# Kernel optimization log

Hardware: AMD Instinct MI355X
Metric: run time of the kernel (lower is better)

The kernel has to match this reference:

```python
import jax, jax.numpy as jnp
import numpy as np

SHAPE = (128, 128, 128)  # (D, H, W), batch_size = 1
N = 100000               # number of active voxels
CONV_CH = [(3, 64), (64, 64), (64, 96), (96, 96), (96, 128), (128, 128),
           (128, 160), (160, 160), (160, 192), (192, 192), (192, 224),
           (224, 224), (224, 256), (256, 256)]


def _lin(c, shape):
    Sz, Sy, Sx = shape
    return ((c[:, 0] * Sz + c[:, 1]) * Sy + c[:, 2]) * Sx + c[:, 3]


def _subm_pairs(coords, shape):
    # Submanifold conv indice pairs: for each active voxel and each of the
    # 27 kernel offsets, the row index of the active neighbor, or -1.
    Sz, Sy, Sx = shape
    n = coords.shape[0]
    grid = np.full(Sz * Sy * Sx, -1, np.int64)  # batch size 1 dense lookup (like self.grid)
    grid[_lin(coords, shape)] = np.arange(n)
    pairs = []
    for dz in (-1, 0, 1):
        for dy in (-1, 0, 1):
            for dx in (-1, 0, 1):
                z = coords[:, 1] + dz
                y = coords[:, 2] + dy
                x = coords[:, 3] + dx
                ok = (z >= 0) & (z < Sz) & (y >= 0) & (y < Sy) & (x >= 0) & (x < Sx)
                nl = ((coords[:, 0] * Sz + z) * Sy + y) * Sx + x
                pairs.append(np.where(ok, grid[np.clip(nl, 0, grid.size - 1)], -1))
    return np.stack(pairs)  # [27, n]


def _pool_structure(coords, shape):
    # SparseMaxPool3d(2,2): output sites = unique coords//2; inv maps each
    # input voxel to its output window.
    ns = tuple(s // 2 for s in shape)
    c2 = coords.copy()
    c2[:, 1:] = c2[:, 1:] // 2
    key = _lin(c2, ns)
    uniq, inv = np.unique(key, return_inverse=True)
    Sz, Sy, Sx = ns
    b = uniq // (Sz * Sy * Sx)
    r = uniq % (Sz * Sy * Sx)
    z = r // (Sy * Sx)
    r = r % (Sy * Sx)
    nc = np.stack([b, z, r // Sx, r % Sx], 1).astype(np.int64)
    return nc, inv, uniq.shape[0], ns


def _build_plan(coors_np):
    # Paired SubMConv3d layers share an indice_key -> same pairs per level.
    coords = coors_np.astype(np.int64)
    shape = SHAPE
    plan = []
    for lvl in range(7):
        p = jnp.asarray(_subm_pairs(coords, shape))
        plan.append(('conv', p))
        plan.append(('conv', p))
        if lvl < 6:
            coords, inv, m, shape = _pool_structure(coords, shape)
            plan.append(('pool', jnp.asarray(inv), m))
    return plan


def _subm_conv(feats, pairs, W):
    # gather -> GEMM -> accumulate, per kernel offset (W: [27, Cin, Cout])
    out = jnp.zeros((feats.shape[0], W.shape[2]), feats.dtype)
    for k in range(27):
        idx = pairs[k]
        g = jnp.where((idx >= 0)[:, None], feats[jnp.clip(idx, 0)], 0.0)
        out = out + g @ W[k]
    return out


def _forward(feats, weights, plan):
    wi = 0
    for step in plan:
        if step[0] == 'conv':
            feats = _subm_conv(feats, step[1], weights[wi])
            wi += 1
        else:
            feats = jax.ops.segment_max(feats, step[1], num_segments=step[2])
    return feats


def setup_inputs() -> dict:
    rng = np.random.default_rng(0)
    lin = rng.choice(SHAPE[0] * SHAPE[1] * SHAPE[2], size=N, replace=False)
    z = lin // (SHAPE[1] * SHAPE[2])
    r = lin % (SHAPE[1] * SHAPE[2])
    coors = np.stack([np.zeros(N, np.int32), z.astype(np.int32),
                      (r // SHAPE[2]).astype(np.int32), (r % SHAPE[2]).astype(np.int32)], 1)
    key = jax.random.key(0)
    keys = jax.random.split(key, len(CONV_CH) + 1)
    inp = {
        'features': jax.random.normal(keys[0], (N, 3), jnp.float32),
        'coors': jnp.asarray(coors),
        'batch_size': 1,
    }
    for i, (ci, co) in enumerate(CONV_CH):
        inp[f'w{i}'] = jax.random.normal(keys[i + 1], (27, ci, co), jnp.float32) * (1.0 / np.sqrt(27.0 * ci))
    return inp


def reference(features, coors, batch_size, w0, w1, w2, w3, w4, w5, w6, w7, w8, w9, w10, w11, w12, w13):
    plan = _build_plan(np.asarray(coors))
    ws = [w0, w1, w2, w3, w4, w5, w6, w7, w8, w9, w10, w11, w12, w13]
    return _forward(features, ws, plan)
```

## Files before the change

### kernel.cpp

```cpp
#include <hip/hip_runtime.h>
#include <cstdint>
#include <cstddef>


typedef __attribute__((ext_vector_type(8))) short short8v;
typedef __attribute__((ext_vector_type(4))) float f32x4;

static inline int cdiv_h(int a, int b) { return (a + b - 1) / b; }

__device__ inline unsigned short f2bf(float f) {
    unsigned int u = __builtin_bit_cast(unsigned int, f);
    u += 0x7FFFu + ((u >> 16) & 1u);
    return (unsigned short)(u >> 16);
}
__device__ inline float bf2f(unsigned short h) {
    unsigned int u = ((unsigned int)h) << 16;
    return __builtin_bit_cast(float, u);
}

__device__ inline void gload_lds16(const void* g, void* l) {
    auto gp = (const __attribute__((address_space(1))) unsigned int*)(uintptr_t)g;
    auto lp = (__attribute__((address_space(3))) unsigned int*)(uintptr_t)l;
    __builtin_amdgcn_global_load_lds(gp, lp, 16, 0, 0);
}

__device__ inline int xcd_swz(int bid, int nwg) {
    int q = nwg >> 3, r = nwg & 7;
    int x = bid & 7, idx = bid >> 3;
    return (x < r ? x * (q + 1) : r * (q + 1) + (x - r) * q) + idx;
}

__global__ void set_count_k(int* counts, int n) { counts[0] = n; }

__global__ void scatter_grid_k(const int* __restrict__ coords, const int* __restrict__ cnt,
                               int* __restrict__ grid, int S)
{
    int i = blockIdx.x * blockDim.x + threadIdx.x;
    if (i >= cnt[0]) return;
    int z = coords[i * 4 + 1], y = coords[i * 4 + 2], x = coords[i * 4 + 3];
    grid[(z * S + y) * S + x] = i;
}

__global__ void build_pairs_k(const int* __restrict__ coords, const int* __restrict__ cnt,
                              const int* __restrict__ grid, int* __restrict__ pairs_t, int S)
{
    int i = blockIdx.x * blockDim.x + threadIdx.x;
    if (i >= cnt[0]) return;
    int z = coords[i * 4 + 1], y = coords[i * 4 + 2], x = coords[i * 4 + 3];
    int4* dst = reinterpret_cast<int4*>(pairs_t + (size_t)i * 32);
#pragma unroll
    for (int g = 0; g < 7; ++g) {
        int4 q;
#pragma unroll
        for (int j = 0; j < 4; ++j) {
            int k = g * 4 + j;
            int v = -1;
            if (k < 27) {
                int nz = z + k / 9 - 1;
                int ny = y + (k / 3) % 3 - 1;
                int nx = x + k % 3 - 1;
                if (nz >= 0 && nz < S && ny >= 0 && ny < S && nx >= 0 && nx < S)
                    v = grid[(nz * S + ny) * S + nx];
            }
            ((int*)&q)[j] = v;
        }
        dst[g] = q;
    }
}

struct PackArgs {
    const float* src[13];
    unsigned short* dst[13];
    int cin[13];
    int cout[13];
    int tileStart[14];
};

__global__ __launch_bounds__(256) void pack_all_k(PackArgs pa)
{
    int g = blockIdx.x * 4 + ((int)threadIdx.x >> 6);
    int lane = (int)threadIdx.x & 63;
    if (g >= pa.tileStart[13]) return;
    int li = 0;
    while (li < 12 && g >= pa.tileStart[li + 1]) ++li;
    int tile = g - pa.tileStart[li];
    int CIN = pa.cin[li], COUT = pa.cout[li];
    int NS = CIN >> 5, NT = COUT >> 4;
    int t = tile % NT;
    int s = (tile / NT) % NS;
    int k = tile / (NT * NS);
    int kabs = s * 32 + (lane >> 4) * 8;
    int c = t * 16 + (lane & 15);
    const float* src = pa.src[li] + ((size_t)(k * CIN + kabs)) * COUT + c;
    unsigned short* dst = pa.dst[li] + (size_t)tile * 512 + lane * 8;
#pragma unroll
    for (int j = 0; j < 8; ++j) dst[j] = f2bf(src[(size_t)j * COUT]);
}

__global__ __launch_bounds__(256) void conv0_k(
    const float* __restrict__ fin, const float* __restrict__ W,
    const int* __restrict__ pairs_t, const int* __restrict__ cnt,
    unsigned short* __restrict__ fout)
{
    const int row = blockIdx.x * 16 + ((int)threadIdx.x >> 4);
    const int cg = ((int)threadIdx.x & 15) * 4;
    if (row >= cnt[0]) return;
    float a0 = 0, a1 = 0, a2 = 0, a3 = 0;
    for (int k = 0; k < 27; ++k) {
        int nb = pairs_t[(size_t)row * 32 + k];
        if (nb < 0) continue;
        const float* fr = fin + (size_t)nb * 3;
        const float* wk = W + (size_t)k * 3 * 64 + cg;
#pragma unroll
        for (int ci = 0; ci < 3; ++ci) {
            float f = fr[ci];
            float4 w = *reinterpret_cast<const float4*>(wk + ci * 64);
            a0 += f * w.x; a1 += f * w.y; a2 += f * w.z; a3 += f * w.w;
        }
    }
    size_t o = (size_t)row * 64 + cg;
    fout[o] = f2bf(a0); fout[o + 1] = f2bf(a1);
    fout[o + 2] = f2bf(a2); fout[o + 3] = f2bf(a3);
}

template <int CIN, int COUT, int RT, int CT, int GY, bool OUTF32>
__global__ __launch_bounds__(256) void conv_lds_k(
    const unsigned short* __restrict__ fin, const unsigned short* __restrict__ Wp,
    const int* __restrict__ pairs_t, const int* __restrict__ cnt,
    void* __restrict__ fout)
{
    constexpr int NS = CIN / 32, NT = COUT / 16;
    constexpr int NCH = NS * CT;
    __shared__ unsigned short sB[2][NCH * 512];

    const int lane = (int)threadIdx.x & 63;
    const int wave = (int)threadIdx.x >> 6;
    const int l15 = lane & 15, lhi = lane >> 4;
    const int M = cnt[0];

    const int lid = xcd_swz((int)blockIdx.x, (int)gridDim.x);
    const int rowBlock = lid / GY;
    const int ct0 = (lid % GY) * CT;
    const int rowBase = (rowBlock * 4 + wave) * (RT * 16);

    const unsigned short* __restrict__ finL = fin + (size_t)lhi * 8;

    f32x4 acc[RT][CT];
#pragma unroll
    for (int a = 0; a < RT; ++a)
#pragma unroll
        for (int b = 0; b < CT; ++b) acc[a][b] = (f32x4){0.f, 0.f, 0.f, 0.f};

    int  rowC[RT];
    bool rOK[RT];
#pragma unroll
    for (int rt = 0; rt < RT; ++rt) {
        int r = rowBase + rt * 16 + l15;
        rOK[rt]  = r < M;
        rowC[rt] = rOK[rt] ? r : 0;
    }

#define STAGE(K, BUF)                                                              \
    {                                                                              \
        const unsigned short* srcB = Wp + (size_t)(K) * (NS * NT * 512)            \
                                     + (size_t)lane * 8;                           \
        _Pragma("unroll") for (int ii = 0; ii < (NCH + 3) / 4; ++ii) {             \
            int idx = wave + ii * 4;                                               \
            if (idx < NCH) {                                                       \
                int s = idx / CT, tt = idx % CT;                                   \
                gload_lds16(srcB + ((size_t)s * NT + ct0 + tt) * 512,              \
                            &sB[BUF][idx * 512]);                                  \
            }                                                                      \
        }                                                                          \
    }

    int nbCur[RT], nbNxt[RT];
#pragma unroll
    for (int rt = 0; rt < RT; ++rt)
        nbCur[rt] = rOK[rt] ? pairs_t[(size_t)rowC[rt] * 32 + 0] : -1;

    STAGE(0, 0);

    for (int k = 0; k < 27; ++k) {
        __syncthreads();
        if (k < 26) {
            STAGE(k + 1, (k + 1) & 1);
#pragma unroll
            for (int rt = 0; rt < RT; ++rt)
                nbNxt[rt] = rOK[rt] ? pairs_t[(size_t)rowC[rt] * 32 + (k + 1)] : -1;
        }

        int nb[RT], act[RT];
        bool anyAct = false;
#pragma unroll
        for (int rt = 0; rt < RT; ++rt) {
            nb[rt] = nbCur[rt];
            act[rt] = __any(nb[rt] >= 0);
            anyAct = anyAct || (act[rt] != 0);
        }
#pragma unroll
        for (int rt = 0; rt < RT; ++rt) nbCur[rt] = nbNxt[rt];

        if (anyAct) {
            const unsigned short* __restrict__ buf = sB[k & 1];
            short8v afr[NS][RT];
#pragma unroll
            for (int s = 0; s < NS; ++s)
#pragma unroll
                for (int rt = 0; rt < RT; ++rt) {
                    afr[s][rt] = (short8v){};
                    if (nb[rt] >= 0)
                        afr[s][rt] = *reinterpret_cast<const short8v*>(
                            finL + (size_t)nb[rt] * CIN + s * 32);
                }
#pragma unroll
            for (int s = 0; s < NS; ++s) {
                short8v bb[CT];
#pragma unroll
                for (int t = 0; t < CT; ++t)
                    bb[t] = *reinterpret_cast<const short8v*>(
                        &buf[(s * CT + t) * 512 + lane * 8]);
#pragma unroll
                for (int rt = 0; rt < RT; ++rt) {
                    if (!act[rt]) continue;
#pragma unroll
                    for (int t = 0; t < CT; ++t)
                        acc[rt][t] = __builtin_amdgcn_mfma_f32_16x16x32_bf16(
                            afr[s][rt], bb[t], acc[rt][t], 0, 0, 0);
                }
            }
        }
    }
#undef STAGE

#pragma unroll
    for (int rt = 0; rt < RT; ++rt) {
#pragma unroll
        for (int j = 0; j < 4; ++j) {
            int r = rowBase + rt * 16 + lhi * 4 + j;
            if (r >= M) continue;
#pragma unroll
            for (int t = 0; t < CT; ++t) {
                int c = (ct0 + t) * 16 + l15;
                if constexpr (OUTF32)
                    ((float*)fout)[(size_t)r * COUT + c] = acc[rt][t][j];
                else
                    ((unsigned short*)fout)[(size_t)r * COUT + c] = f2bf(acc[rt][t][j]);
            }
        }
    }
}

template <int CIN, int COUT, int CTD, int TG>
__global__ __launch_bounds__(64) void conv_deep_k(
    const unsigned short* __restrict__ fin, const unsigned short* __restrict__ Wp,
    const int* __restrict__ pairs_t, const int* __restrict__ cnt,
    float* __restrict__ fout)
{
    constexpr int NS = CIN / 32, NT = COUT / 16;
    const int lane = (int)threadIdx.x;
    const int l15 = lane & 15, lhi = lane >> 4;
    const int M = cnt[0];
    if ((int)blockIdx.x * 16 >= M) return;
    const int row = blockIdx.x * 16 + l15;
    const int ct0 = blockIdx.y * CTD;
    const int k0 = blockIdx.z * TG;

    f32x4 acc[CTD];
#pragma unroll
    for (int t = 0; t < CTD; ++t) acc[t] = (f32x4){0.f, 0.f, 0.f, 0.f};

    bool anyTap = false;
#pragma unroll
    for (int kk = 0; kk < TG; ++kk) {
        const int k = k0 + kk;
        int nb = (row < M) ? pairs_t[(size_t)row * 32 + k] : -1;
        if (!__any(nb >= 0)) continue;
        anyTap = true;
        const unsigned short* wk = Wp + (size_t)k * NS * NT * 512 + (size_t)lane * 8;
#pragma unroll
        for (int s = 0; s < NS; ++s) {
            short8v a = (short8v){};
            if (nb >= 0)
                a = *reinterpret_cast<const short8v*>(
                    fin + (size_t)nb * CIN + s * 32 + lhi * 8);
#pragma unroll
            for (int t = 0; t < CTD; ++t) {
                short8v b = *reinterpret_cast<const short8v*>(
                    wk + ((size_t)s * NT + ct0 + t) * 512);
                acc[t] = __builtin_amdgcn_mfma_f32_16x16x32_bf16(a, b, acc[t], 0, 0, 0);
            }
        }
    }
    if (!anyTap) return;

#pragma unroll
    for (int t = 0; t < CTD; ++t)
#pragma unroll
        for (int j = 0; j < 4; ++j) {
            int r = blockIdx.x * 16 + lhi * 4 + j;
            if (r < M)
                atomicAdd(&fout[(size_t)r * COUT + (ct0 + t) * 16 + l15], acc[t][j]);
        }
}

__global__ __launch_bounds__(256) void f32_to_bf16_k(
    const float* __restrict__ src, const int* __restrict__ cnt,
    unsigned short* __restrict__ dst, int C)
{
    int idx = blockIdx.x * 256 + (int)threadIdx.x;
    if (idx / C >= cnt[0]) return;
    dst[idx] = f2bf(src[idx]);
}

__global__ void mark_occ_k(const int* __restrict__ coords, const int* __restrict__ cnt,
                           int* __restrict__ occ, int Sh)
{
    int i = blockIdx.x * blockDim.x + threadIdx.x;
    if (i >= cnt[0]) return;
    int z = coords[i * 4 + 1] >> 1, y = coords[i * 4 + 2] >> 1, x = coords[i * 4 + 3] >> 1;
    occ[(z * Sh + y) * Sh + x] = 1;
}

__global__ __launch_bounds__(256) void scan_sum_k(const int* __restrict__ occ, int P,
                                                  int* __restrict__ bsum)
{
    int base = blockIdx.x * 4096 + (int)threadIdx.x * 16;
    int s = 0;
#pragma unroll
    for (int j = 0; j < 16; ++j) { int i = base + j; s += (i < P) ? occ[i] : 0; }
    for (int off = 1; off < 64; off <<= 1) s += __shfl_xor(s, off);
    __shared__ int ws[4];
    if ((threadIdx.x & 63) == 0) ws[threadIdx.x >> 6] = s;
    __syncthreads();
    if (threadIdx.x == 0) bsum[blockIdx.x] = ws[0] + ws[1] + ws[2] + ws[3];
}

__global__ void scan_offsets_k(const int* __restrict__ bsum, int nb,
                               int* __restrict__ boff, int* __restrict__ cntOut)
{
    int lane = threadIdx.x;
    int v = (lane < nb) ? bsum[lane] : 0;
    int incl = v;
    for (int off = 1; off < 64; off <<= 1) {
        int t = __shfl_up(incl, off);
        if (lane >= off) incl += t;
    }
    if (lane < nb) boff[lane] = incl - v;
    if (lane == 63) cntOut[0] = incl;
}

__global__ __launch_bounds__(256) void scan_emit_k(const int* __restrict__ occ, int P,
                                                   const int* __restrict__ boff,
                                                   int* __restrict__ newcoords, int Sh)
{
    __shared__ int ws[4];
    int tid = threadIdx.x;
    int base = blockIdx.x * 4096 + tid * 16;
    int v[16];
    int s = 0;
#pragma unroll
    for (int j = 0; j < 16; ++j) { int i = base + j; v[j] = (i < P) ? occ[i] : 0; s += v[j]; }
    int mysum = s;
    int incl = s;
    for (int off = 1; off < 64; off <<= 1) {
        int t = __shfl_up(incl, off);
        if ((tid & 63) >= off) incl += t;
    }
    if ((tid & 63) == 63) ws[tid >> 6] = incl;
    __syncthreads();
    int waveOff = 0;
    for (int w = 0; w < (tid >> 6); ++w) waveOff += ws[w];
    int r = boff[blockIdx.x] + waveOff + incl - mysum;
    const int SS = Sh * Sh;
#pragma unroll
    for (int j = 0; j < 16; ++j) {
        if (v[j]) {
            int c = base + j;
            newcoords[r * 4 + 0] = 0;
            newcoords[r * 4 + 1] = c / SS;
            newcoords[r * 4 + 2] = (c % SS) / Sh;
            newcoords[r * 4 + 3] = c % Sh;
            ++r;
        }
    }
}

__global__ void pool_max_k(const unsigned short* __restrict__ fin, const int* __restrict__ gridPrev,
                           const int* __restrict__ newcoords, const int* __restrict__ cnt,
                           unsigned short* __restrict__ fout, int C, int Sprev)
{
    int idx = blockIdx.x * blockDim.x + threadIdx.x;
    int r = idx / C, c = idx % C;
    if (r >= cnt[0]) return;
    int z2 = newcoords[r * 4 + 1] * 2;
    int y2 = newcoords[r * 4 + 2] * 2;
    int x2 = newcoords[r * 4 + 3] * 2;
    float best = -3.4e38f;
    unsigned short bb = 0;
#pragma unroll
    for (int d = 0; d < 8; ++d) {
        int z = z2 + (d >> 2), y = y2 + ((d >> 1) & 1), x = x2 + (d & 1);
        int j = gridPrev[(z * Sprev + y) * Sprev + x];
        if (j >= 0) {
            unsigned short u = fin[(size_t)j * C + c];
            float f = bf2f(u);
            if (f > best) { best = f; bb = u; }
        }
    }
    fout[(size_t)r * C + c] = bb;
}


template <int CIN, int COUT, int RT, int CT, int GY, bool OUTF32>
static void launch_cl(const unsigned short* fin, const unsigned short* Wp,
                      const int* pairs_t, const int* cnt, void* fout,
                      int bound, hipStream_t stream)
{
    constexpr int NT = COUT / 16;
    static_assert(CIN % 32 == 0 && COUT % 16 == 0 && CT * GY == NT, "shape");
    dim3 g(cdiv_h(bound, RT * 64) * GY);
    conv_lds_k<CIN, COUT, RT, CT, GY, OUTF32><<<g, 256, 0, stream>>>(fin, Wp, pairs_t,
                                                                     cnt, fout);
}

template <int CIN, int COUT, int CTD, int TG>
static void launch_deep(const unsigned short* fin, const unsigned short* Wp,
                        const int* pairs_t, const int* cnt, float* acc,
                        int bound, hipStream_t stream)
{
    constexpr int NT = COUT / 16;
    static_assert(NT % CTD == 0 && 27 % TG == 0, "shape");
    dim3 g(cdiv_h(bound, 16), NT / CTD, 27 / TG);
    conv_deep_k<CIN, COUT, CTD, TG><<<g, 64, 0, stream>>>(fin, Wp, pairs_t, cnt, acc);
}

extern "C" void kernel_launch(void* const* d_in, const int* in_sizes, int n_in,
                              void* d_out, int out_size, void* d_ws, size_t ws_size,
                              hipStream_t stream)
{
    const float* feats0 = (const float*)d_in[0];
    const int*   coors  = (const int*)d_in[1];
    const float* w[14];
    for (int i = 0; i < 14; ++i) w[i] = (const float*)d_in[3 + i];
    float* out = (float*)d_out;
    const int N = in_sizes[0] / 3;

    char* p = (char*)d_ws;
    int* grid   = (int*)p; p += (size_t)128 * 128 * 128 * 4;
    int* occ    = (int*)p; p += (size_t)64 * 64 * 64 * 4;
    int* counts = (int*)p; p += 256;
    int* bsum   = (int*)p; p += 256;
    int* boff   = (int*)p; p += 256;
    int* pairs_t = (int*)p; p += (size_t)N * 32 * 4;
    int* coordsA = (int*)p; p += (size_t)N * 16;
    int* coordsB = (int*)p; p += (size_t)N * 16;
    unsigned short* featA = (unsigned short*)p; p += (size_t)N * 96 * 2;
    unsigned short* featB = (unsigned short*)p; p += (size_t)N * 96 * 2;
    float* scratch = (float*)p; p += (size_t)4096 * 192 * 4;
    unsigned short* wpBase = (unsigned short*)p;

    static const int CH[14][2] = {{3,64},{64,64},{64,96},{96,96},{96,128},{128,128},
                                  {128,160},{160,160},{160,192},{192,192},{192,224},
                                  {224,224},{224,256},{256,256}};
    unsigned short* wp[14];
    PackArgs pa;
    {
        size_t off = 0;
        int ts = 0;
        for (int i = 1; i < 14; ++i) {
            wp[i] = wpBase + off;
            off += (size_t)27 * CH[i][0] * CH[i][1];
            pa.src[i - 1] = w[i];
            pa.dst[i - 1] = wp[i];
            pa.cin[i - 1] = CH[i][0];
            pa.cout[i - 1] = CH[i][1];
            pa.tileStart[i - 1] = ts;
            ts += 27 * (CH[i][0] / 32) * (CH[i][1] / 16);
        }
        pa.tileStart[13] = ts;
    }

    int bounds[7];
    for (int l = 0; l < 7; ++l) {
        int S = 128 >> l, c = S * S * S;
        bounds[l] = N < c ? N : c;
    }

    set_count_k<<<1, 1, 0, stream>>>(counts, N);
    hipMemsetAsync(d_out, 0, (size_t)out_size * 4, stream);
    pack_all_k<<<cdiv_h(pa.tileStart[13], 4), 256, 0, stream>>>(pa);

    auto build_level = [&](const int* coordsL, int lvl) {
        int S = 128 >> lvl;
        hipMemsetAsync(grid, 0xFF, (size_t)S * S * S * 4, stream);
        int blocks = cdiv_h(bounds[lvl], 256);
        scatter_grid_k<<<blocks, 256, 0, stream>>>(coordsL, counts + lvl, grid, S);
        build_pairs_k<<<blocks, 256, 0, stream>>>(coordsL, counts + lvl, grid, pairs_t, S);
    };

    auto do_pool = [&](const int* coordsL, int lvl, const unsigned short* fin,
                       unsigned short* fout, int C, int* coordsOut) {
        int S = 128 >> lvl, Sh = S / 2, P = Sh * Sh * Sh;
        hipMemsetAsync(occ, 0, (size_t)P * 4, stream);
        mark_occ_k<<<cdiv_h(bounds[lvl], 256), 256, 0, stream>>>(coordsL, counts + lvl, occ, Sh);
        int nb = cdiv_h(P, 4096);
        scan_sum_k<<<nb, 256, 0, stream>>>(occ, P, bsum);
        scan_offsets_k<<<1, 64, 0, stream>>>(bsum, nb, boff, counts + lvl + 1);
        scan_emit_k<<<nb, 256, 0, stream>>>(occ, P, boff, coordsOut, Sh);
        int total = bounds[lvl + 1] * C;
        pool_max_k<<<cdiv_h(total, 256), 256, 0, stream>>>(fin, grid, coordsOut,
                                                           counts + lvl + 1, fout, C, S);
    };

    auto deep_conv = [&](auto launcher, const unsigned short* fin, int wi, int lvl,
                         unsigned short* dst, int COUT) {
        hipMemsetAsync(scratch, 0, (size_t)bounds[lvl] * COUT * 4, stream);
        launcher(fin, wp[wi], pairs_t, counts + lvl, scratch, bounds[lvl], stream);
        f32_to_bf16_k<<<cdiv_h(bounds[lvl] * COUT, 256), 256, 0, stream>>>(
            scratch, counts + lvl, dst, COUT);
    };

    build_level(coors, 0);
    conv0_k<<<cdiv_h(bounds[0], 16), 256, 0, stream>>>(feats0, w[0], pairs_t, counts + 0, featA);
    launch_cl<64, 64, 2, 4, 1, false>(featA, wp[1], pairs_t, counts + 0, featB, bounds[0], stream);
    do_pool(coors, 0, featB, featA, 64, coordsA);
    build_level(coordsA, 1);
    launch_cl<64, 96, 2, 6, 1, false>(featA, wp[2], pairs_t, counts + 1, featB, bounds[1], stream);
    launch_cl<96, 96, 2, 6, 1, false>(featB, wp[3], pairs_t, counts + 1, featA, bounds[1], stream);
    do_pool(coordsA, 1, featA, featB, 96, coordsB);
    build_level(coordsB, 2);
    launch_cl<96, 128, 2, 4, 2, false>(featB, wp[4], pairs_t, counts + 2, featA, bounds[2], stream);
    launch_cl<128, 128, 2, 4, 2, false>(featA, wp[5], pairs_t, counts + 2, featB, bounds[2], stream);
    do_pool(coordsB, 2, featB, featA, 128, coordsA);
    build_level(coordsA, 3);
    deep_conv(launch_deep<128, 160, 2, 3>, featA, 6, 3, featB, 160);
    deep_conv(launch_deep<160, 160, 2, 3>, featB, 7, 3, featA, 160);
    do_pool(coordsA, 3, featA, featB, 160, coordsB);
    build_level(coordsB, 4);
    deep_conv(launch_deep<160, 192, 2, 3>, featB, 8, 4, featA, 192);
    deep_conv(launch_deep<192, 192, 2, 3>, featA, 9, 4, featB, 192);
    do_pool(coordsB, 4, featB, featA, 192, coordsA);
    build_level(coordsA, 5);
    deep_conv(launch_deep<192, 224, 1, 1>, featA, 10, 5, featB, 224);
    deep_conv(launch_deep<224, 224, 1, 1>, featB, 11, 5, featA, 224);
    do_pool(coordsA, 5, featA, featB, 224, coordsB);
    build_level(coordsB, 6);
    deep_conv(launch_deep<224, 256, 1, 1>, featB, 12, 6, featA, 256);
    launch_deep<256, 256, 1, 1>(featA, wp[13], pairs_t, counts + 6, out, bounds[6], stream);
}
```

Baseline: 746.5 us.

## Software-pipeline neighbor feature gathers one tap ahead of MFMA compute

The main sparse conv kernel now gathers the next tap's neighbor indices and A-fragments into a second register set while computing the current tap. The 27-tap loop is unrolled by two with ping-pong register arrays, so global gather latency overlaps the MFMA work. The deep-tap kernel also hoists all A loads ahead of its MFMA loop. This roughly doubles the A-fragment registers held at once, which may lower occupancy or cause spills.

Result: slower. 774.7 us (+3.8%).

```diff
diff --git a/kernel.cpp b/kernel.cpp
--- a/kernel.cpp
+++ b/kernel.cpp
@@ -174,64 +174,66 @@
         }                                                                          \
     }
 
-    int nbCur[RT], nbNxt[RT];
-#pragma unroll
-    for (int rt = 0; rt < RT; ++rt)
-        nbCur[rt] = rOK[rt] ? pairs_t[(size_t)rowC[rt] * 32 + 0] : -1;
-
+#define GATHER(AARR, NBARR, KT)                                                    \
+    {                                                                              \
+        _Pragma("unroll") for (int rt = 0; rt < RT; ++rt)                          \
+            NBARR[rt] = rOK[rt] ? pairs_t[(size_t)rowC[rt] * 32 + (KT)] : -1;      \
+        _Pragma("unroll") for (int s = 0; s < NS; ++s)                             \
+        _Pragma("unroll") for (int rt = 0; rt < RT; ++rt) {                        \
+            AARR[s][rt] = (short8v){};                                             \
+            if (NBARR[rt] >= 0)                                                    \
+                AARR[s][rt] = *reinterpret_cast<const short8v*>(                   \
+                    finL + (size_t)NBARR[rt] * CIN + s * 32);                      \
+        }                                                                          \
+    }
+
+#define COMPUTE(AARR, NBARR, BUF)                                                  \
+    {                                                                              \
+        int act[RT]; bool anyAct = false;                                          \
+        _Pragma("unroll") for (int rt = 0; rt < RT; ++rt) {                        \
+            act[rt] = __any(NBARR[rt] >= 0);                                       \
+            anyAct = anyAct || (act[rt] != 0);                                     \
+        }                                                                          \
+        if (anyAct) {                                                              \
+            const unsigned short* __restrict__ buf = sB[BUF];                      \
+            _Pragma("unroll") for (int s = 0; s < NS; ++s) {                       \
+                short8v bb[CT];                                                    \
+                _Pragma("unroll") for (int t = 0; t < CT; ++t)                     \
+                    bb[t] = *reinterpret_cast<const short8v*>(                     \
+                        &buf[(s * CT + t) * 512 + lane * 8]);                      \
+                _Pragma("unroll") for (int rt = 0; rt < RT; ++rt) {                \
+                    if (!act[rt]) continue;                                        \
+                    _Pragma("unroll") for (int t = 0; t < CT; ++t)                 \
+                        acc[rt][t] = __builtin_amdgcn_mfma_f32_16x16x32_bf16(      \
+                            AARR[s][rt], bb[t], acc[rt][t], 0, 0, 0);              \
+                }                                                                  \
+            }                                                                      \
+        }                                                                          \
+    }
+
+    int nbP[RT], nbQ[RT];
+    short8v aP[NS][RT], aQ[NS][RT];
+
+    GATHER(aP, nbP, 0);
     STAGE(0, 0);
 
-    for (int k = 0; k < 27; ++k) {
+    for (int kk = 0; kk < 13; ++kk) {
+        const int k1 = 2 * kk + 1;
         __syncthreads();
-        if (k < 26) {
-            STAGE(k + 1, (k + 1) & 1);
-#pragma unroll
-            for (int rt = 0; rt < RT; ++rt)
-                nbNxt[rt] = rOK[rt] ? pairs_t[(size_t)rowC[rt] * 32 + (k + 1)] : -1;
-        }
-
-        int nb[RT], act[RT];
-        bool anyAct = false;
-#pragma unroll
-        for (int rt = 0; rt < RT; ++rt) {
-            nb[rt] = nbCur[rt];
-            act[rt] = __any(nb[rt] >= 0);
-            anyAct = anyAct || (act[rt] != 0);
-        }
-#pragma unroll
-        for (int rt = 0; rt < RT; ++rt) nbCur[rt] = nbNxt[rt];
-
-        if (anyAct) {
-            const unsigned short* __restrict__ buf = sB[k & 1];
-            short8v afr[NS][RT];
-#pragma unroll
-            for (int s = 0; s < NS; ++s)
-#pragma unroll
-                for (int rt = 0; rt < RT; ++rt) {
-                    afr[s][rt] = (short8v){};
-                    if (nb[rt] >= 0)
-                        afr[s][rt] = *reinterpret_cast<const short8v*>(
-                            finL + (size_t)nb[rt] * CIN + s * 32);
-                }
-#pragma unroll
-            for (int s = 0; s < NS; ++s) {
-                short8v bb[CT];
-#pragma unroll
-                for (int t = 0; t < CT; ++t)
-                    bb[t] = *reinterpret_cast<const short8v*>(
-                        &buf[(s * CT + t) * 512 + lane * 8]);
-#pragma unroll
-                for (int rt = 0; rt < RT; ++rt) {
-                    if (!act[rt]) continue;
-#pragma unroll
-                    for (int t = 0; t < CT; ++t)
-                        acc[rt][t] = __builtin_amdgcn_mfma_f32_16x16x32_bf16(
-                            afr[s][rt], bb[t], acc[rt][t], 0, 0, 0);
-                }
-            }
-        }
-    }
+        STAGE(k1, 1);
+        GATHER(aQ, nbQ, k1);
+        COMPUTE(aP, nbP, 0);
+        __syncthreads();
+        STAGE(k1 + 1, 0);
+        GATHER(aP, nbP, k1 + 1);
+        COMPUTE(aQ, nbQ, 1);
+    }
+    __syncthreads();
+    COMPUTE(aP, nbP, 0);
+
 #undef STAGE
+#undef GATHER
+#undef COMPUTE
 
 #pragma unroll
     for (int rt = 0; rt < RT; ++rt) {
@@ -278,19 +280,23 @@
         if (!__any(nb >= 0)) continue;
         anyTap = true;
         const unsigned short* wk = Wp + (size_t)k * NS * NT * 512 + (size_t)lane * 8;
+
+        short8v a[NS];
 #pragma unroll
         for (int s = 0; s < NS; ++s) {
-            short8v a = (short8v){};
+            a[s] = (short8v){};
             if (nb >= 0)
-                a = *reinterpret_cast<const short8v*>(
+                a[s] = *reinterpret_cast<const short8v*>(
                     fin + (size_t)nb * CIN + s * 32 + lhi * 8);
+        }
+#pragma unroll
+        for (int s = 0; s < NS; ++s)
 #pragma unroll
             for (int t = 0; t < CTD; ++t) {
                 short8v b = *reinterpret_cast<const short8v*>(
                     wk + ((size_t)s * NT + ct0 + t) * 512);
-                acc[t] = __builtin_amdgcn_mfma_f32_16x16x32_bf16(a, b, acc[t], 0, 0, 0);
+                acc[t] = __builtin_amdgcn_mfma_f32_16x16x32_bf16(a[s], b, acc[t], 0, 0, 0);
             }
-        }
     }
     if (!anyTap) return;
 
```
